# Kernel optimization log

Hardware: AMD Instinct MI355X
Metric: run time of the kernel (lower is better)

The kernel has to match this reference:

```python
import jax, jax.numpy as jnp
import numpy as np

B, H, N, T = 16, 16, 4096, 8
D_S, D_ID, L, K = 256, 128, 8, 32
HS, DQ = 8, 32
D_HID = 1024
D_STEER = 3 * D_S + D_ID  # cat(s_cur, id_cur, walker_state, token_embed)


def _gelu(x):
    return jax.nn.gelu(x, approximate=False)


def _rms(x, w):
    return x * jax.lax.rsqrt(jnp.mean(x * x, axis=-1, keepdims=True) + 1e-6) * w


def _mlp2(x, w1, b1, w2, b2):
    return _gelu(x @ w1 + b1) @ w2 + b2


def _per_plane_mlp(x, plane_idx, W1, b1, W2, b2):
    # x: [n, D_in]; plane_idx: [n] int in [0,L). Vectorized plane dispatch:
    # compute all planes then select (avoids data-dependent masking).
    h_all = jnp.einsum('nd,phd->nph', x, W1) + b1[None]          # [n,L,D_hid]
    h = jnp.take_along_axis(h_all, plane_idx[:, None, None], axis=1)[:, 0]
    h = _gelu(h)
    o_all = jnp.einsum('nh,pdh->npd', h, W2) + b2[None]          # [n,L,D_out]
    return jnp.take_along_axis(o_all, plane_idx[:, None, None], axis=1)[:, 0]


def setup_inputs() -> dict:
    key = jax.random.key(0)
    ks = jax.random.split(key, 16)
    f = jax.random.normal
    return {
        's': f(ks[0], (B, N, D_S), jnp.float32),
        'node_id': f(ks[1], (N, D_ID), jnp.float32),
        'walker_state': f(ks[2], (B, H, D_S), jnp.float32),
        'token_embed': f(ks[3], (B, T, D_S), jnp.float32),
        'norm_w': jnp.ones((D_S,), jnp.float32),
        'W1': f(ks[4], (L, D_HID, D_STEER), jnp.float32) * 0.014,
        'b1': jnp.zeros((L, D_HID), jnp.float32),
        'W2': f(ks[5], (L, D_S, D_HID), jnp.float32) * (2.0 / D_HID) ** 0.5,
        'b2': jnp.zeros((L, D_S), jnp.float32),
        'qw1': f(ks[6], (D_STEER, 2 * HS * DQ), jnp.float32) * 0.014,
        'qb1': jnp.zeros((2 * HS * DQ,), jnp.float32),
        'qw2': f(ks[7], (2 * HS * DQ, HS * DQ), jnp.float32) * 0.02,
        'qb2': jnp.zeros((HS * DQ,), jnp.float32),
        'kw1': f(ks[8], (D_ID, 2 * HS * DQ), jnp.float32) * 0.014,
        'kb1': jnp.zeros((2 * HS * DQ,), jnp.float32),
        'kw2': f(ks[9], (2 * HS * DQ, HS * DQ), jnp.float32) * 0.02,
        'kb2': jnp.zeros((HS * DQ,), jnp.float32),
        'walker_pos': jax.random.randint(ks[10], (B, H), 0, N, jnp.int32),
        'plane_idx': jax.random.randint(ks[11], (B, H), 0, L, jnp.int32),
        'neighbors': jax.random.randint(ks[12], (N, K), 0, N, jnp.int32),
    }


def reference(s, node_id, walker_state, token_embed, norm_w, W1, b1, W2, b2,
              qw1, qb1, qw2, qb2, kw1, kb1, kw2, kb2,
              walker_pos, plane_idx, neighbors):
    b_idx = jnp.arange(B)[:, None]            # [B,1] batch gather index
    plane_flat = plane_idx.reshape(-1)        # [B*H], constant per walker
    scale = 1.0 / (HS * np.sqrt(DQ).astype(np.float32))

    def step(carry, tok):
        s, pos, wstate, co, vc, lb = carry
        s_cur = s[b_idx, pos]                 # gather [B,H,D_s]
        id_cur = node_id[pos]                 # [B,H,D_id]
        s_n = _rms(s_cur, norm_w)
        tok_b = jnp.broadcast_to(tok[:, None, :], (B, H, D_S))
        steer = jnp.concatenate([s_n, id_cur, wstate, tok_b], axis=-1)  # [B,H,D_steer]
        # per-plane content MLP (dispatch by plane index)
        content = _per_plane_mlp(steer.reshape(B * H, D_STEER), plane_flat,
                                 W1, b1, W2, b2).reshape(B, H, D_S)
        # shared q/k projections and neighbor scoring
        q = _mlp2(steer, qw1, qb1, qw2, qb2).reshape(B, H, HS, DQ)
        nbr = neighbors[pos]                  # [B,H,K]
        k = _mlp2(node_id[nbr], kw1, kb1, kw2, kb2).reshape(B, H, K, HS, DQ)
        scores = jnp.einsum('bhsd,bhksd->bhk', q, k) * scale   # [B,H,K]
        probs = jax.nn.softmax(scores, axis=-1)
        mp = probs.mean(axis=(0, 1))
        lb = lb + K * jnp.sum(mp * mp)        # load-balance penalty
        # non-differentiable hop: argmax move
        sel = jnp.argmax(scores, axis=-1)     # [B,H]
        next_pos = jnp.take_along_axis(nbr, sel[..., None], axis=-1)[..., 0]
        # state updates: scatter content into s, residual walker state
        s_new = s.at[b_idx, pos].add(content)
        wstate_new = wstate + content
        # non-grad co-visit / visit-count accumulators
        pf = pos.reshape(-1)
        nf = next_pos.reshape(-1)
        co = co.at[pf, nf].add(1.0)
        vc = vc.at[nf].add(1.0)
        motor = wstate_new.mean(axis=1)       # [B,D_s]
        return (s_new, next_pos, wstate_new, co, vc, lb), motor

    init = (s, walker_pos, walker_state,
            jnp.zeros((N, N), jnp.float32), jnp.zeros((N,), jnp.float32),
            jnp.float32(0.0))
    (s_new, pos_new, ws_new, co, vc, lb), motors = jax.lax.scan(
        step, init, token_embed.transpose(1, 0, 2))
    motor_bt = motors.transpose(1, 0, 2)      # [B,T,D_s]
    return motor_bt, s_new, pos_new, ws_new, co, vc, lb
```

## Files before the change

kernel.cpp:

```cpp
#include <hip/hip_runtime.h>
#include <math.h>

#define B_    16
#define H_    16
#define N_    4096
#define T_    8
#define DS_   256
#define DID_  128
#define L_    8
#define K_    32
#define DHID_ 1024
#define DSTEER_ 896
#define QH_   512
#define QO_   256
#define NW_   256
#define SLOTS_ 512
#define BSLD_ 36
#define SCORE_SCALE 0.022097086912079608f

struct KArgs {
    const float *s_in, *node_id, *ws_in, *token, *norm_w;
    const float *W1, *b1, *W2, *b2;
    const float *qw1, *qb1, *qw2, *qb2, *kw1, *kb1, *kw2, *kb2;
    const int *walker_pos, *plane_idx, *neighbors;
    float *out_motor, *out_s, *out_pos, *out_ws, *out_co, *out_vc, *out_lb;
    float *keys, *kh, *qw1T, *qw2T, *h1p, *q1p, *c2p, *q2p, *mp_all;
    int *pos, *plane_order, *chunk_plane, *chunk_rows, *slot_of, *nchunks;
};

__device__ __forceinline__ float gelu_exact(float x) {
    return 0.5f * x * (1.0f + erff(x * 0.70710678118654752f));
}

#define FMA4(c, b, a) { c.x = fmaf(b.x, (a), c.x); c.y = fmaf(b.y, (a), c.y); \
                        c.z = fmaf(b.z, (a), c.z); c.w = fmaf(b.w, (a), c.w); }

__device__ __forceinline__ void gelu4(float4& v) {
    v.x = gelu_exact(v.x); v.y = gelu_exact(v.y);
    v.z = gelu_exact(v.z); v.w = gelu_exact(v.w);
}

__device__ __forceinline__ void rgemm_inner(
    const float* __restrict__ a0, const float* __restrict__ a1,
    const float* bp, int ldb, int K,
    float4& c0, float4& c1)
{
    for (int k = 0; k < K; k += 8) {
        const float4 a0l = *reinterpret_cast<const float4*>(a0 + k);
        const float4 a0h = *reinterpret_cast<const float4*>(a0 + k + 4);
        const float4 a1l = *reinterpret_cast<const float4*>(a1 + k);
        const float4 a1h = *reinterpret_cast<const float4*>(a1 + k + 4);
        const float* b8 = bp + (size_t)k * ldb;
#define KSTEP(o, av0, av1) { float4 bv = *reinterpret_cast<const float4*>(b8 + (size_t)(o) * ldb); \
                             FMA4(c0, bv, av0); FMA4(c1, bv, av1); }
        KSTEP(0, a0l.x, a1l.x)
        KSTEP(1, a0l.y, a1l.y)
        KSTEP(2, a0l.z, a1l.z)
        KSTEP(3, a0l.w, a1l.w)
        KSTEP(4, a0h.x, a1h.x)
        KSTEP(5, a0h.y, a1h.y)
        KSTEP(6, a0h.z, a1h.z)
        KSTEP(7, a0h.w, a1h.w)
#undef KSTEP
    }
}


__global__ __launch_bounds__(256) void setup1_kernel(KArgs a)
{
    int bid = blockIdx.x, tid = threadIdx.x;
    if (bid < 1024) {
        int u = bid;
        int rt = u >> 3, ct = u & 7;
        int tr = tid >> 4, tc = tid & 15;
        int row = rt * 32 + tr * 2, col = ct * 64 + tc * 4;
        const float* a0 = a.node_id + (size_t)row * DID_;
        float4 c0 = {0.f,0.f,0.f,0.f}, c1 = {0.f,0.f,0.f,0.f};
        rgemm_inner(a0, a0 + DID_, a.kw1 + col, QH_, DID_, c0, c1);
        float4 bv = *reinterpret_cast<const float4*>(a.kb1 + col);
        c0.x += bv.x; c0.y += bv.y; c0.z += bv.z; c0.w += bv.w;
        c1.x += bv.x; c1.y += bv.y; c1.z += bv.z; c1.w += bv.w;
        gelu4(c0); gelu4(c1);
        *reinterpret_cast<float4*>(a.kh + (size_t)row * QH_ + col) = c0;
        *reinterpret_cast<float4*>(a.kh + (size_t)(row + 1) * QH_ + col) = c1;
    } else if (bid == 1024) {
        a.pos[tid] = a.walker_pos[tid];
        a.mp_all[tid] = 0.f;
        __shared__ int cnt_s[8];
        __shared__ int cplane_s[16], cbase_s[16];
        __shared__ int nch_s;
        int wave = tid >> 6, lane = tid & 63;
        for (int pp = wave; pp < 8; pp += 4) {
            int base = 0;
            for (int c0 = 0; c0 < NW_; c0 += 64) {
                int w = c0 + lane;
                bool hit = (a.plane_idx[w] == pp);
                unsigned long long mask = __ballot(hit);
                if (hit) {
                    int rank = __popcll(mask & ((1ull << lane) - 1ull));
                    a.plane_order[pp * NW_ + base + rank] = w;
                }
                base += __popcll(mask);
            }
            if (lane == 0) cnt_s[pp] = base;
        }
        __syncthreads();
        if (tid == 0) {
            int nc = 0;
            for (int p = 0; p < 8; ++p)
                for (int s0 = 0; s0 < cnt_s[p]; s0 += 32) {
                    cplane_s[nc] = p; cbase_s[nc] = s0; ++nc;
                }
            *a.nchunks = nc;
            nch_s = nc;
        }
        __syncthreads();
        int nc = nch_s;
        for (int idx = tid; idx < 512; idx += 256) {
            int c = idx >> 5, i = idx & 31;
            int v = -1;
            if (c < nc) {
                int p = cplane_s[c];
                int r = cbase_s[c] + i;
                if (r < cnt_s[p]) v = a.plane_order[p * NW_ + r];
            }
            a.chunk_rows[c * 32 + i] = v;
            if (v >= 0) a.slot_of[v] = c * 32 + i;
            if (i == 0) a.chunk_plane[c] = (c < nc) ? cplane_s[c] : 0;
        }
    } else if (bid < 1601) {
        __shared__ float ts[32][33];
        int u = bid - 1025;
        const float* src; float* dst; int srcld, dstld, td, tj;
        if (u < 448) {
            src = a.qw1; dst = a.qw1T; srcld = QH_; dstld = DSTEER_;
            td = u >> 4; tj = u & 15;
        } else {
            u -= 448;
            src = a.qw2; dst = a.qw2T; srcld = QO_; dstld = QH_;
            td = u >> 3; tj = u & 7;
        }
#pragma unroll
        for (int i = 0; i < 4; ++i) {
            int e = tid + i * 256;
            int r = e >> 5, cc = e & 31;
            ts[r][cc] = src[(size_t)(td * 32 + r) * srcld + tj * 32 + cc];
        }
        __syncthreads();
#pragma unroll
        for (int i = 0; i < 4; ++i) {
            int e = tid + i * 256;
            int r = e >> 5, cc = e & 31;
            dst[(size_t)(tj * 32 + r) * dstld + td * 32 + cc] = ts[cc][r];
        }
    } else {
        int gid = (bid - 1601) * 256 + tid, stride = 2048 * 256;
        float4* s4o = reinterpret_cast<float4*>(a.out_s);
        const float4* s4i = reinterpret_cast<const float4*>(a.s_in);
        for (int i = gid; i < 4194304; i += stride) s4o[i] = s4i[i];
        float4* w4o = reinterpret_cast<float4*>(a.out_ws);
        const float4* w4i = reinterpret_cast<const float4*>(a.ws_in);
        for (int i = gid; i < 16384; i += stride) w4o[i] = w4i[i];
    }
}


__global__ __launch_bounds__(256) void setup2_kernel(KArgs a)
{
    int bid = blockIdx.x, tid = threadIdx.x;
    int rt = bid >> 2, ct = bid & 3;
    int tr = tid >> 4, tc = tid & 15;
    int row = rt * 32 + tr * 2, col = ct * 64 + tc * 4;
    const float* a0 = a.kh + (size_t)row * QH_;
    float4 c0 = {0.f,0.f,0.f,0.f}, c1 = {0.f,0.f,0.f,0.f};
    rgemm_inner(a0, a0 + QH_, a.kw2 + col, QO_, QH_, c0, c1);
    float4 bv = *reinterpret_cast<const float4*>(a.kb2 + col);
    c0.x += bv.x; c0.y += bv.y; c0.z += bv.z; c0.w += bv.w;
    c1.x += bv.x; c1.y += bv.y; c1.z += bv.z; c1.w += bv.w;
    *reinterpret_cast<float4*>(a.keys + (size_t)row * QO_ + col) = c0;
    *reinterpret_cast<float4*>(a.keys + (size_t)(row + 1) * QO_ + col) = c1;
}


__global__ __launch_bounds__(256) void l1_kernel(KArgs a, int t)
{
    __shared__ float bs[224 * BSLD_];
    __shared__ float rms_s[32];
    __shared__ int w_s[32], pos_s[32];
    int bid = blockIdx.x, tid = threadIdx.x;
    int kp, jt, c = -1, p = 0, wt = 0, isQ;
    if (bid < 256) {
        isQ = 1; kp = bid & 3;
        int tile = bid >> 2;
        wt = tile >> 3; jt = tile & 7;
    } else {
        isQ = 0;
        int b2 = bid - 256; kp = b2 & 3;
        int tile = b2 >> 2;
        c = tile >> 4; jt = tile & 15;
        if (c >= *a.nchunks) return;
        p = a.chunk_plane[c];
    }
    int g = tid >> 3, l8 = tid & 7;
    if (l8 == 0) {
        int w = isQ ? (wt * 32 + g) : a.chunk_rows[c * 32 + g];
        w_s[g] = w;
        pos_s[g] = (w >= 0) ? a.pos[w] : 0;
    }
    __syncthreads();
    if (kp < 2) {
        int w = w_s[g];
        float ssum = 0.f;
        if (w >= 0) {
            const float* sr = a.out_s + ((size_t)(w >> 4) * N_ + pos_s[g]) * DS_ + l8 * 32;
#pragma unroll
            for (int i = 0; i < 8; ++i) {
                float4 v = *reinterpret_cast<const float4*>(sr + i * 4);
                ssum += v.x * v.x + v.y * v.y + v.z * v.z + v.w * v.w;
            }
        }
        ssum += __shfl_xor(ssum, 1);
        ssum += __shfl_xor(ssum, 2);
        ssum += __shfl_xor(ssum, 4);
        if (l8 == 0) rms_s[g] = rsqrtf(ssum * (1.0f / DS_) + 1e-6f);
    }
    __syncthreads();
    {
        int w = w_s[g];
        int b = (w >= 0) ? (w >> 4) : 0;
        int pp = pos_s[g];
        float rr = (kp < 2) ? rms_s[g] : 0.f;
#pragma unroll
        for (int i = 0; i < 7; ++i) {
            int kk = l8 * 28 + i * 4;
            int d4 = kp * 224 + kk;
            float4 v = make_float4(0.f, 0.f, 0.f, 0.f);
            if (w >= 0) {
                if (d4 < 256) {
                    float4 sv = *reinterpret_cast<const float4*>(
                        a.out_s + ((size_t)b * N_ + pp) * DS_ + d4);
                    float4 nv = *reinterpret_cast<const float4*>(a.norm_w + d4);
                    v.x = sv.x * rr * nv.x; v.y = sv.y * rr * nv.y;
                    v.z = sv.z * rr * nv.z; v.w = sv.w * rr * nv.w;
                } else if (d4 < 384) {
                    v = *reinterpret_cast<const float4*>(
                        a.node_id + (size_t)pp * DID_ + (d4 - 256));
                } else if (d4 < 640) {
                    v = *reinterpret_cast<const float4*>(
                        a.out_ws + (size_t)w * DS_ + (d4 - 384));
                } else {
                    v = *reinterpret_cast<const float4*>(
                        a.token + ((size_t)b * T_ + t) * DS_ + (d4 - 640));
                }
            }
            bs[(kk + 0) * BSLD_ + g] = v.x;
            bs[(kk + 1) * BSLD_ + g] = v.y;
            bs[(kk + 2) * BSLD_ + g] = v.z;
            bs[(kk + 3) * BSLD_ + g] = v.w;
        }
    }
    __syncthreads();
    int tr = tid >> 3, tc = tid & 7;
    float4 c0 = {0.f,0.f,0.f,0.f}, c1 = {0.f,0.f,0.f,0.f};
    if (isQ) {
        int j = jt * 64 + tr * 2;
        const float* a0 = a.qw1T + (size_t)j * DSTEER_ + kp * 224;
        rgemm_inner(a0, a0 + DSTEER_, bs + tc * 4, BSLD_, 224, c0, c1);
        float* o = a.q1p + (size_t)kp * 131072;
        int w4 = wt * 32 + tc * 4;
        *reinterpret_cast<float4*>(o + (size_t)j * NW_ + w4) = c0;
        *reinterpret_cast<float4*>(o + (size_t)(j + 1) * NW_ + w4) = c1;
    } else {
        int J = jt * 64 + tr * 2;
        const float* a0 = a.W1 + ((size_t)p * DHID_ + J) * DSTEER_ + kp * 224;
        rgemm_inner(a0, a0 + DSTEER_, bs + tc * 4, BSLD_, 224, c0, c1);
        float* o = a.h1p + (size_t)kp * 524288;
        int slot = c * 32 + tc * 4;
        *reinterpret_cast<float4*>(o + (size_t)J * SLOTS_ + slot) = c0;
        *reinterpret_cast<float4*>(o + (size_t)(J + 1) * SLOTS_ + slot) = c1;
    }
}


__global__ __launch_bounds__(256) void l2f_kernel(KArgs a)
{
    __shared__ float smem[4224];
    int bid = blockIdx.x, tid = threadIdx.x;
    if (bid < 256) {
        int kp = bid & 7, tile = bid >> 3;
        int colt = tile >> 3, wt = tile & 7;
#pragma unroll
        for (int i = 0; i < 8; ++i) {
            int idx = tid + i * 256;
            int hh = idx >> 5, wl = idx & 31;
            size_t off = (size_t)(kp * 64 + hh) * NW_ + wt * 32 + wl;
            float acc = a.qb1[kp * 64 + hh];
#pragma unroll
            for (int p4 = 0; p4 < 4; ++p4) acc += a.q1p[(size_t)p4 * 131072 + off];
            smem[hh * 32 + wl] = gelu_exact(acc);
        }
        __syncthreads();
        int tr = tid >> 3, tc = tid & 7;
        int col = colt * 64 + tr * 2;
        const float* a0 = a.qw2T + (size_t)col * QH_ + kp * 64;
        float4 c0 = {0.f,0.f,0.f,0.f}, c1 = {0.f,0.f,0.f,0.f};
        rgemm_inner(a0, a0 + QH_, smem + tc * 4, 32, 64, c0, c1);
        __syncthreads();
        int cl = tr * 2;
        smem[(tc*4+0)*66 + cl]     = c0.x;
        smem[(tc*4+1)*66 + cl]     = c0.y;
        smem[(tc*4+2)*66 + cl]     = c0.z;
        smem[(tc*4+3)*66 + cl]     = c0.w;
        smem[(tc*4+0)*66 + cl + 1] = c1.x;
        smem[(tc*4+1)*66 + cl + 1] = c1.y;
        smem[(tc*4+2)*66 + cl + 1] = c1.z;
        smem[(tc*4+3)*66 + cl + 1] = c1.w;
        __syncthreads();
        float* o = a.q2p + (size_t)kp * 65536;
#pragma unroll
        for (int i = 0; i < 2; ++i) {
            int f4i = tid + i * 256;
            int wl = f4i >> 4, j4 = (f4i & 15) << 2;
            float4 v;
            v.x = smem[wl * 66 + j4 + 0];
            v.y = smem[wl * 66 + j4 + 1];
            v.z = smem[wl * 66 + j4 + 2];
            v.w = smem[wl * 66 + j4 + 3];
            *reinterpret_cast<float4*>(o + (size_t)(wt * 32 + wl) * QO_ + colt * 64 + j4) = v;
        }
    } else {
        int b2i = bid - 256;
        int kp = b2i & 7, tile = b2i >> 3;
        int c = tile >> 2, jt = tile & 3;
        if (c >= *a.nchunks) return;
        int p = a.chunk_plane[c];
        int tr = tid >> 3, tc = tid & 7;
        int J = jt * 64 + tr * 2;
        float4 c0 = {0.f,0.f,0.f,0.f}, c1 = {0.f,0.f,0.f,0.f};
#pragma unroll
        for (int i = 0; i < 4; ++i) {
            int idx = tid + i * 256;
            int kk = idx >> 3, s4 = (idx & 7) << 2;
            int kq = kp * 128 + kk;
            size_t off = (size_t)kq * SLOTS_ + c * 32 + s4;
            float bj = a.b1[p * DHID_ + kq];
            float4 acc = {bj, bj, bj, bj};
#pragma unroll
            for (int p4 = 0; p4 < 4; ++p4) {
                float4 v = *reinterpret_cast<const float4*>(a.h1p + (size_t)p4 * 524288 + off);
                acc.x += v.x; acc.y += v.y; acc.z += v.z; acc.w += v.w;
            }
            gelu4(acc);
            *reinterpret_cast<float4*>(smem + kk * 32 + s4) = acc;
        }
        __syncthreads();
        const float* a0 = a.W2 + ((size_t)p * DS_ + J) * DHID_ + kp * 128;
        rgemm_inner(a0, a0 + DHID_, smem + tc * 4, 32, 128, c0, c1);
        __syncthreads();
        int jl = tr * 2;
        smem[(tc*4+0)*66 + jl]     = c0.x;
        smem[(tc*4+1)*66 + jl]     = c0.y;
        smem[(tc*4+2)*66 + jl]     = c0.z;
        smem[(tc*4+3)*66 + jl]     = c0.w;
        smem[(tc*4+0)*66 + jl + 1] = c1.x;
        smem[(tc*4+1)*66 + jl + 1] = c1.y;
        smem[(tc*4+2)*66 + jl + 1] = c1.z;
        smem[(tc*4+3)*66 + jl + 1] = c1.w;
        __syncthreads();
        float* o = a.c2p + (size_t)kp * 131072;
#pragma unroll
        for (int i = 0; i < 2; ++i) {
            int f4i = tid + i * 256;
            int sl = f4i >> 4, j4 = (f4i & 15) << 2;
            float4 v;
            v.x = smem[sl * 66 + j4 + 0];
            v.y = smem[sl * 66 + j4 + 1];
            v.z = smem[sl * 66 + j4 + 2];
            v.w = smem[sl * 66 + j4 + 3];
            *reinterpret_cast<float4*>(o + (size_t)(c * 32 + sl) * 256 + jt * 64 + j4) = v;
        }
    }
}


__global__ __launch_bounds__(256) void score_kernel(KArgs a, int t)
{
    int w = blockIdx.x;
    int b = w >> 4;
    int tid = threadIdx.x;
    int pold = a.pos[w];
    int slot = a.slot_of[w];
    __shared__ float qv_s[256];
    __shared__ int nbr_s[32];
    __shared__ float part_s[8][32];
    __shared__ float sc_s[32];
    if (tid < 32) nbr_s[tid] = a.neighbors[(size_t)pold * K_ + tid];
    float qsum = a.qb2[tid];
#pragma unroll
    for (int kp = 0; kp < 8; ++kp) qsum += a.q2p[(size_t)kp * 65536 + (size_t)w * QO_ + tid];
    qv_s[tid] = qsum;
    float csum = a.b2[a.chunk_plane[slot >> 5] * DS_ + tid];
#pragma unroll
    for (int kp = 0; kp < 8; ++kp) csum += a.c2p[(size_t)kp * 131072 + (size_t)slot * 256 + tid];
    __syncthreads();
    int k = tid & 31, part = tid >> 5;
    int nk = nbr_s[k];
    const float* kp_ = a.keys + (size_t)nk * 256 + part * 32;
    const float* qp = qv_s + part * 32;
    float acc = 0.f;
#pragma unroll
    for (int i = 0; i < 32; i += 4) {
        float4 kv = *reinterpret_cast<const float4*>(kp_ + i);
        acc += kv.x * qp[i] + kv.y * qp[i+1] + kv.z * qp[i+2] + kv.w * qp[i+3];
    }
    part_s[part][k] = acc;
    __syncthreads();
    if (tid < 32) {
        float s = 0.f;
#pragma unroll
        for (int p8 = 0; p8 < 8; ++p8) s += part_s[p8][tid];
        sc_s[tid] = s * SCORE_SCALE;
    }
    __syncthreads();
    if (tid < 32) {
        float sv = sc_s[tid];
        float m = sv;
        for (int off = 1; off < 32; off <<= 1) m = fmaxf(m, __shfl_xor(m, off));
        float e = expf(sv - m);
        float ssum = e;
        for (int off = 1; off < 32; off <<= 1) ssum += __shfl_xor(ssum, off);
        float prob = e / ssum;
        atomicAdd(&a.mp_all[t * 32 + tid], prob);
        float bs = sv; int bi = tid;
        for (int off = 1; off < 32; off <<= 1) {
            float os = __shfl_xor(bs, off);
            int   oi = __shfl_xor(bi, off);
            if (os > bs || (os == bs && oi < bi)) { bs = os; bi = oi; }
        }
        if (tid == 0) {
            int next = nbr_s[bi];
            a.pos[w] = next;
            if (t == T_ - 1) a.out_pos[w] = (float)next;
            atomicAdd(&a.out_co[(size_t)pold * N_ + next], 1.0f);
            atomicAdd(&a.out_vc[next], 1.0f);
        }
    }
    atomicAdd(&a.out_s[((size_t)b * N_ + pold) * DS_ + tid], csum);
    float wn = a.out_ws[(size_t)w * DS_ + tid] + csum;
    a.out_ws[(size_t)w * DS_ + tid] = wn;
    atomicAdd(&a.out_motor[((size_t)b * T_ + t) * DS_ + tid], wn * (1.0f / H_));
}

__global__ __launch_bounds__(256) void final_kernel(KArgs a)
{
    int tid = threadIdx.x;
    float v = a.mp_all[tid] * (1.0f / 256.f);
    v = v * v;
    for (int off = 32; off > 0; off >>= 1) v += __shfl_down(v, off);
    __shared__ float red[4];
    if ((tid & 63) == 0) red[tid >> 6] = v;
    __syncthreads();
    if (tid == 0) a.out_lb[0] = (float)K_ * (red[0] + red[1] + red[2] + red[3]);
}


extern "C" void kernel_launch(void* const* d_in, const int* in_sizes, int n_in,
                              void* d_out, int out_size, void* d_ws, size_t ws_size,
                              hipStream_t stream)
{
    KArgs a;
    a.s_in    = (const float*)d_in[0];
    a.node_id = (const float*)d_in[1];
    a.ws_in   = (const float*)d_in[2];
    a.token   = (const float*)d_in[3];
    a.norm_w  = (const float*)d_in[4];
    a.W1  = (const float*)d_in[5];
    a.b1  = (const float*)d_in[6];
    a.W2  = (const float*)d_in[7];
    a.b2  = (const float*)d_in[8];
    a.qw1 = (const float*)d_in[9];
    a.qb1 = (const float*)d_in[10];
    a.qw2 = (const float*)d_in[11];
    a.qb2 = (const float*)d_in[12];
    a.kw1 = (const float*)d_in[13];
    a.kb1 = (const float*)d_in[14];
    a.kw2 = (const float*)d_in[15];
    a.kb2 = (const float*)d_in[16];
    a.walker_pos = (const int*)d_in[17];
    a.plane_idx  = (const int*)d_in[18];
    a.neighbors  = (const int*)d_in[19];

    float* out = (float*)d_out;
    a.out_motor = out;
    a.out_s     = a.out_motor + 32768;
    a.out_pos   = a.out_s + (size_t)16777216;
    a.out_ws    = a.out_pos + 256;
    a.out_co    = a.out_ws + 65536;
    a.out_vc    = a.out_co + (size_t)16777216;
    a.out_lb    = a.out_vc + 4096;

    float* ws = (float*)d_ws;
    a.keys   = ws;
    a.qw1T   = a.keys + 1048576;
    a.qw2T   = a.qw1T + 458752;
    a.h1p    = a.qw2T + 131072;
    a.kh     = a.h1p;
    a.q1p    = a.h1p + 2097152;
    a.c2p    = a.q1p + 524288;
    a.q2p    = a.c2p + 1048576;
    a.mp_all = a.q2p + 524288;
    a.pos         = (int*)(a.mp_all + 256);
    a.plane_order = a.pos + 256;
    a.chunk_plane = a.plane_order + 2048;
    a.chunk_rows  = a.chunk_plane + 16;
    a.slot_of     = a.chunk_rows + 512;
    a.nchunks     = a.slot_of + 256;

    hipMemsetAsync(a.out_motor, 0, 32768 * sizeof(float), stream);
    hipMemsetAsync(a.out_co, 0, (size_t)(16777216 + 4096 + 1) * sizeof(float), stream);

    setup1_kernel<<<1024 + 1 + 576 + 2048, 256, 0, stream>>>(a);
    setup2_kernel<<<512, 256, 0, stream>>>(a);
    for (int t = 0; t < T_; ++t) {
        l1_kernel<<<256 + 1024, 256, 0, stream>>>(a, t);
        l2f_kernel<<<768, 256, 0, stream>>>(a);
        score_kernel<<<256, 256, 0, stream>>>(a, t);
    }
    final_kernel<<<1, 256, 0, stream>>>(a);
}
```

Baseline: 485.9 us.

## Fuse two-layer key MLP into single setup kernel via shared-memory hidden tile

The key-path MLP (node_id -> kw1 -> GELU -> kw2) was two kernels with an intermediate kh buffer in global memory. It is now computed in one set of 512 blocks, each handling 8 nodes and keeping the 8x512 hidden activations in LDS. This removes one kernel launch and the global round-trip of the hidden tensor. In exchange each block re-reads the full kw1 and kw2 weights with a simpler, less register-tiled inner loop, so per-block compute efficiency may drop and LDS use per block rises.

```diff
diff --git a/kernel.cpp b/kernel.cpp
--- a/kernel.cpp
+++ b/kernel.cpp
@@ -24,7 +24,7 @@
     const float *qw1, *qb1, *qw2, *qb2, *kw1, *kb1, *kw2, *kb2;
     const int *walker_pos, *plane_idx, *neighbors;
     float *out_motor, *out_s, *out_pos, *out_ws, *out_co, *out_vc, *out_lb;
-    float *keys, *kh, *qw1T, *qw2T, *h1p, *q1p, *c2p, *q2p, *mp_all;
+    float *keys, *qw1T, *qw2T, *h1p, *q1p, *c2p, *q2p, *mp_all;
     int *pos, *plane_order, *chunk_plane, *chunk_rows, *slot_of, *nchunks;
 };
 
@@ -69,21 +69,55 @@
 __global__ __launch_bounds__(256) void setup1_kernel(KArgs a)
 {
     int bid = blockIdx.x, tid = threadIdx.x;
-    if (bid < 1024) {
-        int u = bid;
-        int rt = u >> 3, ct = u & 7;
-        int tr = tid >> 4, tc = tid & 15;
-        int row = rt * 32 + tr * 2, col = ct * 64 + tc * 4;
-        const float* a0 = a.node_id + (size_t)row * DID_;
-        float4 c0 = {0.f,0.f,0.f,0.f}, c1 = {0.f,0.f,0.f,0.f};
-        rgemm_inner(a0, a0 + DID_, a.kw1 + col, QH_, DID_, c0, c1);
-        float4 bv = *reinterpret_cast<const float4*>(a.kb1 + col);
-        c0.x += bv.x; c0.y += bv.y; c0.z += bv.z; c0.w += bv.w;
-        c1.x += bv.x; c1.y += bv.y; c1.z += bv.z; c1.w += bv.w;
-        gelu4(c0); gelu4(c1);
-        *reinterpret_cast<float4*>(a.kh + (size_t)row * QH_ + col) = c0;
-        *reinterpret_cast<float4*>(a.kh + (size_t)(row + 1) * QH_ + col) = c1;
-    } else if (bid == 1024) {
+    if (bid < 512) {
+        __shared__ float id_s[8 * 128];
+        __shared__ float hs[8 * 512];
+        int n0 = bid * 8;
+        {
+            int r = tid >> 5, d4 = (tid & 31) << 2;
+            *reinterpret_cast<float4*>(id_s + r * 128 + d4) =
+                *reinterpret_cast<const float4*>(a.node_id + (size_t)(n0 + r) * DID_ + d4);
+        }
+        __syncthreads();
+        {
+            int j0 = tid * 2;
+            float acc0[8], acc1[8];
+#pragma unroll
+            for (int n = 0; n < 8; ++n) { acc0[n] = 0.f; acc1[n] = 0.f; }
+            for (int d = 0; d < 128; ++d) {
+                float2 wv = *reinterpret_cast<const float2*>(a.kw1 + (size_t)d * QH_ + j0);
+#pragma unroll
+                for (int n = 0; n < 8; ++n) {
+                    float idv = id_s[n * 128 + d];
+                    acc0[n] = fmaf(idv, wv.x, acc0[n]);
+                    acc1[n] = fmaf(idv, wv.y, acc1[n]);
+                }
+            }
+            float b0 = a.kb1[j0], b1v = a.kb1[j0 + 1];
+#pragma unroll
+            for (int n = 0; n < 8; ++n) {
+                hs[n * 512 + j0]     = gelu_exact(acc0[n] + b0);
+                hs[n * 512 + j0 + 1] = gelu_exact(acc1[n] + b1v);
+            }
+        }
+        __syncthreads();
+        {
+            int o = tid;
+            float acc[8];
+#pragma unroll
+            for (int n = 0; n < 8; ++n) acc[n] = 0.f;
+            for (int h = 0; h < 512; ++h) {
+                float wv = a.kw2[(size_t)h * QO_ + o];
+#pragma unroll
+                for (int n = 0; n < 8; ++n)
+                    acc[n] = fmaf(hs[n * 512 + h], wv, acc[n]);
+            }
+            float bo = a.kb2[o];
+#pragma unroll
+            for (int n = 0; n < 8; ++n)
+                a.keys[(size_t)(n0 + n) * QO_ + o] = acc[n] + bo;
+        }
+    } else if (bid == 512) {
         a.pos[tid] = a.walker_pos[tid];
         a.mp_all[tid] = 0.f;
         __shared__ int cnt_s[8];
@@ -128,9 +162,9 @@
             if (v >= 0) a.slot_of[v] = c * 32 + i;
             if (i == 0) a.chunk_plane[c] = (c < nc) ? cplane_s[c] : 0;
         }
-    } else if (bid < 1601) {
+    } else if (bid < 1089) {
         __shared__ float ts[32][33];
-        int u = bid - 1025;
+        int u = bid - 513;
         const float* src; float* dst; int srcld, dstld, td, tj;
         if (u < 448) {
             src = a.qw1; dst = a.qw1T; srcld = QH_; dstld = DSTEER_;
@@ -154,7 +188,7 @@
             dst[(size_t)(tj * 32 + r) * dstld + td * 32 + cc] = ts[cc][r];
         }
     } else {
-        int gid = (bid - 1601) * 256 + tid, stride = 2048 * 256;
+        int gid = (bid - 1089) * 256 + tid, stride = 2048 * 256;
         float4* s4o = reinterpret_cast<float4*>(a.out_s);
         const float4* s4i = reinterpret_cast<const float4*>(a.s_in);
         for (int i = gid; i < 4194304; i += stride) s4o[i] = s4i[i];
@@ -162,23 +196,6 @@
         const float4* w4i = reinterpret_cast<const float4*>(a.ws_in);
         for (int i = gid; i < 16384; i += stride) w4o[i] = w4i[i];
     }
-}
-
-
-__global__ __launch_bounds__(256) void setup2_kernel(KArgs a)
-{
-    int bid = blockIdx.x, tid = threadIdx.x;
-    int rt = bid >> 2, ct = bid & 3;
-    int tr = tid >> 4, tc = tid & 15;
-    int row = rt * 32 + tr * 2, col = ct * 64 + tc * 4;
-    const float* a0 = a.kh + (size_t)row * QH_;
-    float4 c0 = {0.f,0.f,0.f,0.f}, c1 = {0.f,0.f,0.f,0.f};
-    rgemm_inner(a0, a0 + QH_, a.kw2 + col, QO_, QH_, c0, c1);
-    float4 bv = *reinterpret_cast<const float4*>(a.kb2 + col);
-    c0.x += bv.x; c0.y += bv.y; c0.z += bv.z; c0.w += bv.w;
-    c1.x += bv.x; c1.y += bv.y; c1.z += bv.z; c1.w += bv.w;
-    *reinterpret_cast<float4*>(a.keys + (size_t)row * QO_ + col) = c0;
-    *reinterpret_cast<float4*>(a.keys + (size_t)(row + 1) * QO_ + col) = c1;
 }
 
 
@@ -504,7 +521,6 @@
     a.qw1T   = a.keys + 1048576;
     a.qw2T   = a.qw1T + 458752;
     a.h1p    = a.qw2T + 131072;
-    a.kh     = a.h1p;
     a.q1p    = a.h1p + 2097152;
     a.c2p    = a.q1p + 524288;
     a.q2p    = a.c2p + 1048576;
@@ -519,8 +535,7 @@
     hipMemsetAsync(a.out_motor, 0, 32768 * sizeof(float), stream);
     hipMemsetAsync(a.out_co, 0, (size_t)(16777216 + 4096 + 1) * sizeof(float), stream);
 
-    setup1_kernel<<<1024 + 1 + 576 + 2048, 256, 0, stream>>>(a);
-    setup2_kernel<<<512, 256, 0, stream>>>(a);
+    setup1_kernel<<<512 + 1 + 576 + 2048, 256, 0, stream>>>(a);
     for (int t = 0; t < T_; ++t) {
         l1_kernel<<<256 + 1024, 256, 0, stream>>>(a, t);
         l2f_kernel<<<768, 256, 0, stream>>>(a);
```

Result: faster. 455.6 us (-6.2%).
